# Kernel tuning notes

Hardware: AMD Instinct MI355X
Metric: run time of the kernel (lower is better)

## Reference

```python
import jax, jax.numpy as jnp
import numpy as np


def setup_inputs() -> dict:
    key = jax.random.key(0)
    k1, k2 = jax.random.split(key)
    x = jax.random.normal(k1, (32, 512, 2048), dtype=jnp.float32)
    codebook = jax.random.normal(k2, (1024, 512), dtype=jnp.float32)
    return {"x": x, "codebook": codebook}


def reference(x, codebook):
    # x: [N, width, T], codebook: [nb_code, code_dim], width == code_dim
    N, width, T = x.shape
    nb_code = codebook.shape[0]
    # preprocess: [N, width, T] -> [N*T, width]
    xf = jnp.transpose(x, (0, 2, 1)).reshape(-1, width)
    dist = (jnp.sum(xf * xf, axis=-1, keepdims=True)
            - 2.0 * jnp.matmul(xf, codebook.T)
            + jnp.sum(codebook * codebook, axis=-1)[None, :])
    code_idx = jnp.argmin(dist, axis=-1)  # [N*T]
    # dequantize (embedding gather)
    x_d = codebook[code_idx]  # [N*T, width]
    # perplexity over code usage histogram
    counts = jax.ops.segment_sum(jnp.ones(code_idx.shape, dtype=x.dtype),
                                 code_idx, num_segments=nb_code)
    prob = counts / jnp.sum(counts)
    perplexity = jnp.exp(-jnp.sum(prob * jnp.log(prob + 1e-7)))
    # commitment loss against detached quantized vectors
    commit_loss = jnp.mean((xf - jax.lax.stop_gradient(x_d)) ** 2)
    # straight-through estimator
    out = xf + jax.lax.stop_gradient(x_d - xf)
    out = out.reshape(N, T, width).transpose(0, 2, 1)  # [N, width, T]
    return out, code_idx.reshape(N, T), commit_loss, perplexity
```

## Files before the change

### kernel.cpp

```cpp
#include <hip/hip_runtime.h>
#include <cstddef>
#include <cstdint>

#define N_BATCH 32
#define WIDTH   512
#define T_DIM   2048
#define NB_CODE 1024
#define M_ROWS  65536
#define OUT_ELEMS 33554432
#define IDX_OFF  OUT_ELEMS
#define LOSS_OFF (OUT_ELEMS + M_ROWS)
#define PERP_OFF (LOSS_OFF + 1)
#define MARGIN   0.75f

typedef __attribute__((ext_vector_type(8))) short vshort8;
typedef __attribute__((ext_vector_type(4))) float vfloat4;
typedef __attribute__((ext_vector_type(16))) float vfloat16;

typedef __attribute__((address_space(1))) const uint32_t gu32_t;
typedef __attribute__((address_space(3))) uint32_t lu32_t;
static __device__ __forceinline__ void gload16(const void* g, void* l) {
    __builtin_amdgcn_global_load_lds((gu32_t*)g, (lu32_t*)l, 16, 0, 0);
}

static __device__ __forceinline__ unsigned short f2bf(float f) {
    uint32_t u = __float_as_uint(f);
    uint32_t r = (u + 0x7FFFu + ((u >> 16) & 1u)) >> 16;
    return (unsigned short)r;
}
static __device__ __forceinline__ float bf2f(unsigned short s) {
    return __uint_as_float(((uint32_t)s) << 16);
}


__global__ __launch_bounds__(128) void k_prep(const float* __restrict__ cb,
                                              unsigned short* __restrict__ cbh,
                                              float* __restrict__ cnorm,
                                              int* __restrict__ hist) {
    const int c = blockIdx.x, tid = threadIdx.x;
    float4 v = ((const float4*)(cb + (size_t)c * WIDTH))[tid];
    ushort4 h;
    h.x = f2bf(v.x); h.y = f2bf(v.y); h.z = f2bf(v.z); h.w = f2bf(v.w);
    ((ushort4*)(cbh + (size_t)c * WIDTH))[tid] = h;
    float s = v.x * v.x + v.y * v.y + v.z * v.z + v.w * v.w;
#pragma unroll
    for (int off = 32; off >= 1; off >>= 1) s += __shfl_xor(s, off, 64);
    __shared__ float sw[2];
    if ((tid & 63) == 0) sw[tid >> 6] = s;
    __syncthreads();
    if (tid == 0) { cnorm[c] = sw[0] + sw[1]; hist[c] = 0; }
}

__global__ __launch_bounds__(512, 2) void k_argmin(
    const float* __restrict__ x, const unsigned short* __restrict__ cbh,
    const float* __restrict__ cnorm, uint32_t* __restrict__ cand,
    float* __restrict__ sbest, float* __restrict__ xnorm) {
    __shared__ __align__(16) short lds[2][32768];
    __shared__ __align__(16) float cns[NB_CODE];

    const int tid = threadIdx.x;
    const int wv = tid >> 6, l = tid & 63;
    const int l31 = l & 31, hi = l >> 5;
    const int m = l31 & 15;

    int srcoff[8];
#pragma unroll
    for (int j = 0; j < 8; ++j) {
        const int q = wv * 512 + j * 64 + l;
        const int kb = q >> 10, code = (q >> 4) & 63, s = q & 15;
        srcoff[j] = code * 1024 + kb * 256 + ((s ^ (code & 15)) << 4);
    }

#define STAGE(SP, B) do {                                                     \
    const char* cbbase_ = ((const char*)cbh) + (SP) * 65536;                  \
    short* lb_ = &lds[B][0];                                                  \
    _Pragma("unroll")                                                         \
    for (int j = 0; j < 8; ++j)                                               \
        gload16(cbbase_ + srcoff[j], lb_ + (wv * 512 + j * 64) * 8);          \
} while (0)

    STAGE(0, 0);

    { ((float2*)cns)[tid] = ((const float2*)cnorm)[tid]; }

    const int m0w = blockIdx.x * 256 + wv * 32;
    const int n = m0w >> 11;
    const int tcol = (m0w & 2047) + l31;
    vshort8 xh[32];
    float xn = 0.f;
    {
        const float* xb = x + (size_t)n * WIDTH * T_DIM + (size_t)hi * 8 * T_DIM + tcol;
        union U8 { uint32_t u[4]; vshort8 v; };
#pragma unroll
        for (int ks = 0; ks < 32; ++ks) {
            U8 u;
#pragma unroll
            for (int j = 0; j < 4; ++j) {
                const float f0 = xb[(size_t)(ks * 16 + 2 * j) * T_DIM];
                const float f1 = xb[(size_t)(ks * 16 + 2 * j + 1) * T_DIM];
                xn = fmaf(f0, f0, fmaf(f1, f1, xn));
                asm("v_cvt_pk_bf16_f32 %0, %1, %2" : "=v"(u.u[j]) : "v"(f0), "v"(f1));
            }
            xh[ks] = u.v;
        }
    }
    xn += __shfl_xor(xn, 32, 64);
    if (l < 32) xnorm[m0w + l] = xn;

    const int B34 = (m >> 1) << 4;
    const int base_s = l31 * 128 + ((hi ^ (m & 1)) << 3);

    float b1 = 3.4e38f, b2 = 3.4e38f, b3 = 3.4e38f;
    int i1 = 0, i2 = 0, i3 = 0;

#define INS3(S, C) do {                                                       \
        const bool lt1 = (S) < b1, lt2 = (S) < b2, lt3 = (S) < b3;            \
        b3 = lt3 ? (lt2 ? b2 : (S)) : b3;  i3 = lt3 ? (lt2 ? i2 : (C)) : i3; \
        b2 = lt2 ? (lt1 ? b1 : (S)) : b2;  i2 = lt2 ? (lt1 ? i1 : (C)) : i2; \
        b1 = lt1 ? (S) : b1;               i1 = lt1 ? (C) : i1;              \
    } while (0)

    __syncthreads();

    for (int sp = 0; sp < 16; ++sp) {
        if (sp) {
            asm volatile("s_waitcnt vmcnt(0)" ::: "memory");
            __builtin_amdgcn_s_barrier();
        }
        if (sp < 15) {
            if (sp & 1) STAGE(sp + 1, 0); else STAGE(sp + 1, 1);
        }
        const short* buf = lds[sp & 1];
        vfloat16 acc0 = {}, acc1 = {};
        __builtin_amdgcn_s_setprio(1);
#pragma unroll
        for (int ks = 0; ks < 32; ++ks) {
            const int koff = ((ks >> 3) << 13) + (((ks & 7) << 4) ^ B34);
            vshort8 a0 = *(const vshort8*)&buf[base_s + koff];
            acc0 = __builtin_amdgcn_mfma_f32_32x32x16_bf16(a0, xh[ks], acc0, 0, 0, 0);
            vshort8 a1 = *(const vshort8*)&buf[base_s + koff + 4096];
            acc1 = __builtin_amdgcn_mfma_f32_32x32x16_bf16(a1, xh[ks], acc1, 0, 0, 0);
        }
        __builtin_amdgcn_s_setprio(0);
        const int cb0 = sp * 64;
#pragma unroll
        for (int tl = 0; tl < 2; ++tl) {
#pragma unroll
            for (int g = 0; g < 4; ++g) {
                const int cbase = cb0 + tl * 32 + g * 8 + 4 * hi;
                vfloat4 cn = *(const vfloat4*)&cns[cbase];
#pragma unroll
                for (int j = 0; j < 4; ++j) {
                    const float a = tl ? acc1[g * 4 + j] : acc0[g * 4 + j];
                    const float s = fmaf(-2.f, a, cn[j]);
                    INS3(s, cbase + j);
                }
            }
        }
    }

    {
        const float ob1 = __shfl_xor(b1, 32, 64), ob2 = __shfl_xor(b2, 32, 64), ob3 = __shfl_xor(b3, 32, 64);
        const int oi1 = __shfl_xor(i1, 32, 64), oi2 = __shfl_xor(i2, 32, 64), oi3 = __shfl_xor(i3, 32, 64);
        INS3(ob1, oi1); INS3(ob2, oi2); INS3(ob3, oi3);
    }
    if (l < 32) {
        const uint32_t f2 = (b2 - b1 < MARGIN) ? 1u : 0u;
        const uint32_t f3 = (b3 - b1 < MARGIN) ? 1u : 0u;
        cand[m0w + l] = (uint32_t)i1 | ((uint32_t)i2 << 10) | ((uint32_t)i3 << 20) | (f2 << 30) | (f3 << 31);
        sbest[m0w + l] = b1;
    }
}

__global__ __launch_bounds__(256) void k_tail(
    const float* __restrict__ x, const float* __restrict__ cb,
    const float* __restrict__ cnorm, const uint32_t* __restrict__ cand,
    const float* __restrict__ sbest, const float* __restrict__ xnorm,
    float* __restrict__ dout, int* __restrict__ hist,
    float* __restrict__ lossPart) {
    __shared__ int sidx[64];
    __shared__ float sls[64];
    __shared__ int list[64];
    __shared__ int cnt;
    __shared__ float tile[64][130];
    const int tid = threadIdx.x;
    const int b = blockIdx.x;
    const int m0 = b * 64;
    if (tid == 0) cnt = 0;
    __syncthreads();
    if (tid < 64) {
        const uint32_t wv = cand[m0 + tid];
        sidx[tid] = (int)(wv & 1023u);
        sls[tid] = xnorm[m0 + tid] + sbest[m0 + tid];
        if (wv >> 30) { const int p = atomicAdd(&cnt, 1); list[p] = tid; }
    }
    __syncthreads();
    const int nf = cnt;
    const int w = tid >> 6, lid = tid & 63;
    for (int it = w; it < nf; it += 4) {
        const int row = m0 + list[it];
        const uint32_t wv = cand[row];
        const int j1 = (int)(wv & 1023u), j2 = (int)((wv >> 10) & 1023u), j3 = (int)((wv >> 20) & 1023u);
        const bool nd3 = (wv >> 31) & 1u;
        const int n = row >> 11, t = row & 2047;
        const float* xc = x + (size_t)n * WIDTH * T_DIM + t;
        float xv[8];
#pragma unroll
        for (int e = 0; e < 8; ++e)
            xv[e] = xc[(size_t)(lid * 8 + e) * T_DIM];
        float d1 = 0.f, d2 = 0.f, d3 = 0.f;
        {
            const float* c1 = cb + (size_t)j1 * WIDTH + lid * 8;
            const float* c2 = cb + (size_t)j2 * WIDTH + lid * 8;
            const float* c3 = cb + (size_t)j3 * WIDTH + lid * 8;
            float4 a0 = *(const float4*)c1, a1 = *(const float4*)(c1 + 4);
            d1 = fmaf(xv[0], a0.x, fmaf(xv[1], a0.y, fmaf(xv[2], a0.z, fmaf(xv[3], a0.w,
                 fmaf(xv[4], a1.x, fmaf(xv[5], a1.y, fmaf(xv[6], a1.z, xv[7] * a1.w)))))));
            float4 b0 = *(const float4*)c2, b1v = *(const float4*)(c2 + 4);
            d2 = fmaf(xv[0], b0.x, fmaf(xv[1], b0.y, fmaf(xv[2], b0.z, fmaf(xv[3], b0.w,
                 fmaf(xv[4], b1v.x, fmaf(xv[5], b1v.y, fmaf(xv[6], b1v.z, xv[7] * b1v.w)))))));
            if (nd3) {
                float4 g0 = *(const float4*)c3, g1 = *(const float4*)(c3 + 4);
                d3 = fmaf(xv[0], g0.x, fmaf(xv[1], g0.y, fmaf(xv[2], g0.z, fmaf(xv[3], g0.w,
                     fmaf(xv[4], g1.x, fmaf(xv[5], g1.y, fmaf(xv[6], g1.z, xv[7] * g1.w)))))));
            }
        }
#pragma unroll
        for (int off = 32; off >= 1; off >>= 1) {
            d1 += __shfl_xor(d1, off, 64);
            d2 += __shfl_xor(d2, off, 64);
            d3 += __shfl_xor(d3, off, 64);
        }
        if (lid == 0) {
            int win = j1;
            float qw = fmaf(-2.f, d1, cnorm[j1]);
            const float q2 = fmaf(-2.f, d2, cnorm[j2]);
            if (q2 < qw || (q2 == qw && j2 < win)) { win = j2; qw = q2; }
            if (nd3) {
                const float q3 = fmaf(-2.f, d3, cnorm[j3]);
                if (q3 < qw || (q3 == qw && j3 < win)) { win = j3; qw = q3; }
            }
            sidx[list[it]] = win;
            sls[list[it]] = xnorm[row] + qw;
        }
    }
    __syncthreads();
    if (tid < 64) {
        dout[IDX_OFF + m0 + tid] = (float)sidx[tid];
        atomicAdd(&hist[sidx[tid]], 1);
        float ls = sls[tid];
#pragma unroll
        for (int off = 32; off >= 1; off >>= 1) ls += __shfl_xor(ls, off, 64);
        if (tid == 0) lossPart[b] = ls;
    }
    const int n = b >> 5;
    const int t0 = (b & 31) * 64;
    const int l = tid & 63;
    for (int wc = 0; wc < 4; ++wc) {
#pragma unroll
        for (int rr = 0; rr < 16; ++rr) {
            const int row = w * 16 + rr;
            const float2 v = *(const float2*)(cb + (size_t)sidx[row] * WIDTH + wc * 128 + l * 2);
            *(float2*)&tile[row][l * 2] = v;
        }
        __syncthreads();
#pragma unroll 8
        for (int wwi = 0; wwi < 32; ++wwi) {
            const int ww = wc * 128 + w * 32 + wwi;
            dout[((size_t)n * WIDTH + ww) * T_DIM + t0 + l] = tile[l][w * 32 + wwi];
        }
        __syncthreads();
    }
}

__global__ __launch_bounds__(1024) void k_fin(
    const int* __restrict__ hist, const float* __restrict__ lossPart,
    float* __restrict__ dout) {
    const int tid = threadIdx.x;
    const float p = (float)hist[tid] * (1.0f / (float)M_ROWS);
    float e = p * logf(p + 1e-7f);
    float ls = lossPart[tid];
#pragma unroll
    for (int off = 32; off >= 1; off >>= 1) {
        e += __shfl_xor(e, off, 64);
        ls += __shfl_xor(ls, off, 64);
    }
    __shared__ float se[16], sl[16];
    if ((tid & 63) == 0) { se[tid >> 6] = e; sl[tid >> 6] = ls; }
    __syncthreads();
    if (tid == 0) {
        float E = 0.f, L = 0.f;
#pragma unroll
        for (int i = 0; i < 16; ++i) { E += se[i]; L += sl[i]; }
        dout[LOSS_OFF] = L / (float)OUT_ELEMS;
        dout[PERP_OFF] = expf(-E);
    }
}

extern "C" void kernel_launch(void* const* d_in, const int* in_sizes, int n_in,
                              void* d_out, int out_size, void* d_ws, size_t ws_size,
                              hipStream_t stream) {
    const float* x = (const float*)d_in[0];
    const float* cb = (const float*)d_in[1];
    float* dout = (float*)d_out;
    uint8_t* w = (uint8_t*)d_ws;

    unsigned short* cbh = (unsigned short*)w;
    float* cnorm   = (float*)(w + (1u << 20));
    int*   hist    = (int*)(w + (1u << 20) + 4096);
    uint32_t* cand = (uint32_t*)(w + (1u << 20) + 8192);
    float* sbest   = (float*)(w + (1u << 20) + 8192 + 262144);
    float* xnorm   = (float*)(w + (1u << 20) + 8192 + 2 * 262144);
    float* lossPart= (float*)(w + (1u << 20) + 8192 + 3 * 262144);

    k_prep<<<NB_CODE, 128, 0, stream>>>(cb, cbh, cnorm, hist);
    k_argmin<<<M_ROWS / 256, 512, 0, stream>>>(x, cbh, cnorm, cand, sbest, xnorm);
    k_tail<<<1024, 256, 0, stream>>>(x, cb, cnorm, cand, sbest, xnorm, dout, hist, lossPart);
    k_fin<<<1, 1024, 0, stream>>>(hist, lossPart, dout);
}
```

Measured before the change: 171.0 us.

## Shrink argmin blocks to 4 waves with 32-code stages

The argmin kernel now uses 256-thread blocks, each covering 128 rows, and streams the bf16 codebook in 32-code stages (32 stages instead of 16) with a new LDS swizzle and a single MFMA accumulator per wave. The codebook-norm LDS copy is removed and norms are read straight from global memory. The aim is a smaller LDS footprint and more resident blocks per CU. The cost is twice as many codebook stages, each with its own barrier, and half the MFMA work between syncs, which lowers the compute each staged tile is reused for.

```diff
diff --git a/kernel.cpp b/kernel.cpp
--- a/kernel.cpp
+++ b/kernel.cpp
@@ -28,9 +28,6 @@
     uint32_t r = (u + 0x7FFFu + ((u >> 16) & 1u)) >> 16;
     return (unsigned short)r;
 }
-static __device__ __forceinline__ float bf2f(unsigned short s) {
-    return __uint_as_float(((uint32_t)s) << 16);
-}
 
 
 __global__ __launch_bounds__(128) void k_prep(const float* __restrict__ cb,
@@ -51,39 +48,36 @@
     if (tid == 0) { cnorm[c] = sw[0] + sw[1]; hist[c] = 0; }
 }
 
-__global__ __launch_bounds__(512, 2) void k_argmin(
+__global__ __launch_bounds__(256, 2) void k_argmin(
     const float* __restrict__ x, const unsigned short* __restrict__ cbh,
     const float* __restrict__ cnorm, uint32_t* __restrict__ cand,
     float* __restrict__ sbest, float* __restrict__ xnorm) {
-    __shared__ __align__(16) short lds[2][32768];
-    __shared__ __align__(16) float cns[NB_CODE];
+    __shared__ __align__(16) short lds[2][16384];
 
     const int tid = threadIdx.x;
     const int wv = tid >> 6, l = tid & 63;
     const int l31 = l & 31, hi = l >> 5;
-    const int m = l31 & 15;
 
     int srcoff[8];
 #pragma unroll
     for (int j = 0; j < 8; ++j) {
-        const int q = wv * 512 + j * 64 + l;
-        const int kb = q >> 10, code = (q >> 4) & 63, s = q & 15;
+        const int q = j * 256 + tid;
+        const int code = q >> 6, w = q & 63;
+        const int kb = w >> 4, s = w & 15;
         srcoff[j] = code * 1024 + kb * 256 + ((s ^ (code & 15)) << 4);
     }
 
 #define STAGE(SP, B) do {                                                     \
-    const char* cbbase_ = ((const char*)cbh) + (SP) * 65536;                  \
+    const char* cbbase_ = ((const char*)cbh) + (size_t)(SP) * 32768;          \
     short* lb_ = &lds[B][0];                                                  \
     _Pragma("unroll")                                                         \
     for (int j = 0; j < 8; ++j)                                               \
-        gload16(cbbase_ + srcoff[j], lb_ + (wv * 512 + j * 64) * 8);          \
+        gload16(cbbase_ + srcoff[j], lb_ + (j * 256 + tid) * 8);              \
 } while (0)
 
     STAGE(0, 0);
 
-    { ((float2*)cns)[tid] = ((const float2*)cnorm)[tid]; }
-
-    const int m0w = blockIdx.x * 256 + wv * 32;
+    const int m0w = blockIdx.x * 128 + wv * 32;
     const int n = m0w >> 11;
     const int tcol = (m0w & 2047) + l31;
     vshort8 xh[32];
@@ -107,8 +101,8 @@
     xn += __shfl_xor(xn, 32, 64);
     if (l < 32) xnorm[m0w + l] = xn;
 
-    const int B34 = (m >> 1) << 4;
-    const int base_s = l31 * 128 + ((hi ^ (m & 1)) << 3);
+    const int sxl = l31 & 15;
+    const int rbase = l31 * 512;
 
     float b1 = 3.4e38f, b2 = 3.4e38f, b3 = 3.4e38f;
     int i1 = 0, i2 = 0, i3 = 0;
@@ -122,39 +116,34 @@
 
     __syncthreads();
 
-    for (int sp = 0; sp < 16; ++sp) {
+    for (int sp = 0; sp < 32; ++sp) {
         if (sp) {
             asm volatile("s_waitcnt vmcnt(0)" ::: "memory");
             __builtin_amdgcn_s_barrier();
         }
-        if (sp < 15) {
+        if (sp < 31) {
             if (sp & 1) STAGE(sp + 1, 0); else STAGE(sp + 1, 1);
         }
         const short* buf = lds[sp & 1];
-        vfloat16 acc0 = {}, acc1 = {};
+        vfloat16 acc = {};
         __builtin_amdgcn_s_setprio(1);
 #pragma unroll
         for (int ks = 0; ks < 32; ++ks) {
-            const int koff = ((ks >> 3) << 13) + (((ks & 7) << 4) ^ B34);
-            vshort8 a0 = *(const vshort8*)&buf[base_s + koff];
-            acc0 = __builtin_amdgcn_mfma_f32_32x32x16_bf16(a0, xh[ks], acc0, 0, 0, 0);
-            vshort8 a1 = *(const vshort8*)&buf[base_s + koff + 4096];
-            acc1 = __builtin_amdgcn_mfma_f32_32x32x16_bf16(a1, xh[ks], acc1, 0, 0, 0);
+            const int addr = rbase + (ks >> 3) * 128 +
+                             (((((ks & 7) << 1) | hi) ^ sxl) << 3);
+            vshort8 a = *(const vshort8*)&buf[addr];
+            acc = __builtin_amdgcn_mfma_f32_32x32x16_bf16(a, xh[ks], acc, 0, 0, 0);
         }
         __builtin_amdgcn_s_setprio(0);
-        const int cb0 = sp * 64;
-#pragma unroll
-        for (int tl = 0; tl < 2; ++tl) {
-#pragma unroll
-            for (int g = 0; g < 4; ++g) {
-                const int cbase = cb0 + tl * 32 + g * 8 + 4 * hi;
-                vfloat4 cn = *(const vfloat4*)&cns[cbase];
-#pragma unroll
-                for (int j = 0; j < 4; ++j) {
-                    const float a = tl ? acc1[g * 4 + j] : acc0[g * 4 + j];
-                    const float s = fmaf(-2.f, a, cn[j]);
-                    INS3(s, cbase + j);
-                }
+        const int cb0 = sp * 32;
+#pragma unroll
+        for (int g = 0; g < 4; ++g) {
+            const int cbase = cb0 + g * 8 + 4 * hi;
+            const vfloat4 cn = *(const vfloat4*)&cnorm[cbase];
+#pragma unroll
+            for (int j = 0; j < 4; ++j) {
+                const float s = fmaf(-2.f, acc[g * 4 + j], cn[j]);
+                INS3(s, cbase + j);
             }
         }
     }
@@ -314,7 +303,7 @@
     float* lossPart= (float*)(w + (1u << 20) + 8192 + 3 * 262144);
 
     k_prep<<<NB_CODE, 128, 0, stream>>>(cb, cbh, cnorm, hist);
-    k_argmin<<<M_ROWS / 256, 512, 0, stream>>>(x, cbh, cnorm, cand, sbest, xnorm);
+    k_argmin<<<M_ROWS / 128, 256, 0, stream>>>(x, cbh, cnorm, cand, sbest, xnorm);
     k_tail<<<1024, 256, 0, stream>>>(x, cb, cnorm, cand, sbest, xnorm, dout, hist, lossPart);
     k_fin<<<1, 1024, 0, stream>>>(hist, lossPart, dout);
 }
```

New measurement: 162.5 us. -5.0%, faster.
